# Kernel optimization log

Hardware: AMD Instinct MI355X
Metric: run time of the kernel (lower is better)

Reference implementation:

```python
import jax, jax.numpy as jnp
import numpy as np

# config
L, N, D, H, I = 4, 16, 64, 1024, 4096   # layers, heads, head_dim, hidden, intermediate
V, P = 50257, 8192                       # vocab, positions
B, S = 2, 2048                           # batch, seq
EPS = 1e-5


def setup_inputs() -> dict:
    key = jax.random.key(0)
    ks = jax.random.split(key, 20)
    std = 0.02
    inp = {
        "input_ids": jax.random.randint(ks[0], (B, S), 0, V),
        "position_ids": jnp.broadcast_to(jnp.arange(S), (B, S)),
        "wte": jax.random.normal(ks[1], (V, H), jnp.float32) * std,
        "wpe": jax.random.normal(ks[2], (P, H), jnp.float32) * std,
        # per-layer stacked params; torch Linear weights are (out, in)
        "ln1_w": jnp.ones((L, H), jnp.float32),
        "ln1_b": jnp.zeros((L, H), jnp.float32),
        "cattn_w": jax.random.normal(ks[3], (L, H + 2 * D, H), jnp.float32) * std,
        "cattn_b": jnp.zeros((L, H + 2 * D), jnp.float32),
        "cproj_w": jax.random.normal(ks[4], (L, H, H), jnp.float32) * std,
        "cproj_b": jnp.zeros((L, H), jnp.float32),
        "ln2_w": jnp.ones((L, H), jnp.float32),
        "ln2_b": jnp.zeros((L, H), jnp.float32),
        "fc_w": jax.random.normal(ks[5], (L, I, H), jnp.float32) * std,
        "fc_b": jnp.zeros((L, I), jnp.float32),
        "mproj_w": jax.random.normal(ks[6], (L, H, I), jnp.float32) * std,
        "mproj_b": jnp.zeros((L, H), jnp.float32),
        "lnf_w": jnp.ones((H,), jnp.float32),
        "lnf_b": jnp.zeros((H,), jnp.float32),
    }
    return inp


def _ln(x, w, b):
    mu = jnp.mean(x, axis=-1, keepdims=True)
    var = jnp.mean(jnp.square(x - mu), axis=-1, keepdims=True)
    return (x - mu) * jax.lax.rsqrt(var + EPS) * w + b


def _forward(input_ids, position_ids, wte, wpe, ln1_w, ln1_b, cattn_w, cattn_b,
             cproj_w, cproj_b, ln2_w, ln2_b, fc_w, fc_b, mproj_w, mproj_b,
             lnf_w, lnf_b):
    h = wte[input_ids] + wpe[position_ids]              # [B,S,H]
    b, s, _ = h.shape
    causal = jnp.tril(jnp.ones((s, s), bool))[None, :, None, :]   # [1,S,1,S] keep-mask
    neg = jnp.finfo(jnp.float32).min
    for l in range(L):
        # --- attention ---
        resid = h
        x = _ln(h, ln1_w[l], ln1_b[l])
        qkv = x @ cattn_w[l].T + cattn_b[l]             # [B,S,H+2D]
        q = qkv[..., :H].reshape(b, s, N, D)
        k = qkv[..., H:H + D]                           # [B,S,D] shared key head
        v = qkv[..., H + D:]                            # [B,S,D] shared value head
        unscale = float(l + 1)
        scale = 1.0 / (unscale * np.sqrt(D))
        scores = jnp.einsum('bsnd,btd->bsnt', q, k) * scale
        # upcast_masked_softmax: to fp32, re-multiply by unscale, mask, softmax
        scores = scores.astype(jnp.float32) * unscale
        scores = jnp.where(causal, scores, neg)
        attn = jax.nn.softmax(scores, axis=-1).astype(h.dtype)
        out = jnp.einsum('bsnt,btd->bsnd', attn, v).reshape(b, s, H)
        h = resid + (out @ cproj_w[l].T + cproj_b[l])
        # --- mlp ---
        resid = h
        x = _ln(h, ln2_w[l], ln2_b[l])
        x = jax.nn.gelu(x @ fc_w[l].T + fc_b[l], approximate=False)
        h = resid + (x @ mproj_w[l].T + mproj_b[l])
    return _ln(h, lnf_w, lnf_b)


def reference(input_ids, position_ids, wte, wpe, ln1_w, ln1_b, cattn_w, cattn_b,
              cproj_w, cproj_b, ln2_w, ln2_b, fc_w, fc_b, mproj_w, mproj_b,
              lnf_w, lnf_b):
    return _forward(input_ids, position_ids, wte, wpe, ln1_w, ln1_b, cattn_w,
                    cattn_b, cproj_w, cproj_b, ln2_w, ln2_b, fc_w, fc_b,
                    mproj_w, mproj_b, lnf_w, lnf_b)
```

## Files before the change

### kernel.cpp

```cpp
#include <hip/hip_runtime.h>
#include <math.h>

typedef __attribute__((ext_vector_type(8))) short short8;
typedef __attribute__((ext_vector_type(8))) __bf16 bf16x8;
typedef __attribute__((ext_vector_type(4))) float f32x4;

static constexpr int H = 1024, LNUM = 4, SEQ = 2048, BATCH = 2;
static constexpr int TOK = BATCH * SEQ;
static constexpr int NI = 4096, QKVD = H + 128;

__device__ __forceinline__ short f2bf(float f) {
  union { float f; unsigned u; } c; c.f = f;
  return (short)((c.u + 0x7fffu + ((c.u >> 16) & 1u)) >> 16);
}

__device__ __forceinline__ void gl_lds16(const short* g, short* l) {
  __builtin_amdgcn_global_load_lds(
      (const __attribute__((address_space(1))) unsigned*)g,
      (__attribute__((address_space(3))) unsigned*)l, 16, 0, 0);
}

#define MFMA16(a, b, c) __builtin_amdgcn_mfma_f32_16x16x32_bf16(a, b, c, 0, 0, 0)

__global__ __launch_bounds__(256) void embed_kernel(
    const int* __restrict__ ids, const int* __restrict__ pos,
    const float* __restrict__ wte, const float* __restrict__ wpe,
    float* __restrict__ h) {
  int i = blockIdx.x * 256 + threadIdx.x;
  int tok = i >> 10, d = i & 1023;
  h[i] = wte[(size_t)ids[tok] * H + d] + wpe[(size_t)pos[tok] * H + d];
}

__global__ __launch_bounds__(256) void cast_kernel(
    const float* __restrict__ src, short* __restrict__ dst) {
  int i = blockIdx.x * 256 + threadIdx.x;
  float4 v = ((const float4*)src)[i];
  union { short s[4]; uint2 u; } p;
  p.s[0] = f2bf(v.x); p.s[1] = f2bf(v.y); p.s[2] = f2bf(v.z); p.s[3] = f2bf(v.w);
  ((uint2*)dst)[i] = p.u;
}

template <bool BF16_OUT>
__global__ __launch_bounds__(256) void ln_kernel(
    const float* __restrict__ X, const float* __restrict__ w,
    const float* __restrict__ b, void* __restrict__ out) {
  int row = blockIdx.x;
  const float* x = X + (size_t)row * H;
  int tid = threadIdx.x, lane = tid & 63, wid = tid >> 6;
  float v[4];
#pragma unroll
  for (int i = 0; i < 4; i++) v[i] = x[tid + i * 256];
  float s = v[0] + v[1] + v[2] + v[3];
#pragma unroll
  for (int off = 32; off > 0; off >>= 1) s += __shfl_xor(s, off);
  __shared__ float red[8];
  if (lane == 0) red[wid] = s;
  __syncthreads();
  float mu = (red[0] + red[1] + red[2] + red[3]) * (1.0f / H);
  float q = 0.f;
#pragma unroll
  for (int i = 0; i < 4; i++) { float d = v[i] - mu; q += d * d; }
#pragma unroll
  for (int off = 32; off > 0; off >>= 1) q += __shfl_xor(q, off);
  if (lane == 0) red[4 + wid] = q;
  __syncthreads();
  float var = (red[4] + red[5] + red[6] + red[7]) * (1.0f / H);
  float inv = rsqrtf(var + 1e-5f);
#pragma unroll
  for (int i = 0; i < 4; i++) {
    int col = tid + i * 256;
    float r = (v[i] - mu) * inv * w[col] + b[col];
    if (BF16_OUT) ((short*)out)[(size_t)row * H + col] = f2bf(r);
    else          ((float*)out)[(size_t)row * H + col] = r;
  }
}

template <int MODE>
__global__ __launch_bounds__(256) void gemm_mfma(
    const short* __restrict__ A, const short* __restrict__ W,
    const float* __restrict__ bias, void* __restrict__ Cv,
    int M, int N, int K) {
  __shared__ short As[128 * 32];
  __shared__ short Bs[128 * 32];
  int tid = threadIdx.x, wave = tid >> 6, lane = tid & 63;
  int li = lane & 15, lg = lane >> 4;
  int row0 = blockIdx.y * 128, col0 = blockIdx.x * 128;
  int wm = (wave & 1) * 64, wn = (wave >> 1) * 64;
  f32x4 acc[4][4] = {};
  const short* Ab = A + (size_t)(row0 + (tid >> 2)) * K + (tid & 3) * 8;
  const short* Wb = W + (size_t)(col0 + (tid >> 2)) * K + (tid & 3) * 8;
  for (int k0 = 0; k0 < K; k0 += 32) {
    __syncthreads();
    gl_lds16(Ab + k0,            As + tid * 8);
    gl_lds16(Ab + k0 + 64 * K,   As + 2048 + tid * 8);
    gl_lds16(Wb + k0,            Bs + tid * 8);
    gl_lds16(Wb + k0 + 64 * K,   Bs + 2048 + tid * 8);
    __syncthreads();
    bf16x8 af[4], bfr[4];
#pragma unroll
    for (int i = 0; i < 4; ++i) {
      af[i]  = *(const bf16x8*)&As[(wm + i * 16 + li) * 32 + lg * 8];
      bfr[i] = *(const bf16x8*)&Bs[(wn + i * 16 + li) * 32 + lg * 8];
    }
#pragma unroll
    for (int i = 0; i < 4; ++i)
#pragma unroll
      for (int j = 0; j < 4; ++j) acc[i][j] = MFMA16(af[i], bfr[j], acc[i][j]);
  }
  float* Cf = (float*)Cv;
  short* Cs = (short*)Cv;
#pragma unroll
  for (int i = 0; i < 4; ++i) {
    int gr = row0 + wm + i * 16 + lg * 4;
#pragma unroll
    for (int j = 0; j < 4; ++j) {
      int gc = col0 + wn + j * 16 + li;
      float bv = bias[gc];
#pragma unroll
      for (int r = 0; r < 4; ++r) {
        float v = acc[i][j][r] + bv;
        size_t idx = (size_t)(gr + r) * N + gc;
        if (MODE == 1) {
          Cf[idx] += v;
        } else if (MODE == 2) {
          v = 0.5f * v * (1.0f + erff(v * 0.70710678118654752f));
          Cs[idx] = f2bf(v);
        } else {
          Cs[idx] = f2bf(v);
        }
      }
    }
  }
}

__global__ __launch_bounds__(256) void mqa_attn(
    const short* __restrict__ qkv, short* __restrict__ out) {
  int head = blockIdx.x, qt = blockIdx.y, b = blockIdx.z;
  int tid = threadIdx.x, wave = tid >> 6, lane = tid & 63;
  int li = lane & 15, lg = lane >> 4;

  __shared__ short Kc[64 * 72];
  __shared__ short VT[64 * 72];
  __shared__ short Ps[4 * 16 * 72];

  const size_t qrow0 = (size_t)(b * SEQ + qt * 64);
  bf16x8 qf[2];
  {
    const short* qp = qkv + (qrow0 + wave * 16 + li) * QKVD + head * 64 + lg * 8;
    qf[0] = *(const bf16x8*)(qp);
    qf[1] = *(const bf16x8*)(qp + 32);
  }
  f32x4 oacc[4] = {};
  float m_i[4], l_i[4];
#pragma unroll
  for (int r = 0; r < 4; ++r) { m_i[r] = -1e30f; l_i[r] = 0.f; }

  int t_ = tid >> 3, c_ = tid & 7;
  for (int j = 0; j <= qt; ++j) {
    __syncthreads();
    {
      const short* g0 = qkv + ((size_t)(b * SEQ + j * 64 + t_)) * QKVD;
      const short* g1 = g0 + 32 * QKVD;
      short8 k0 = *(const short8*)(g0 + 1024 + c_ * 8);
      short8 k1 = *(const short8*)(g1 + 1024 + c_ * 8);
      short8 v0 = *(const short8*)(g0 + 1088 + c_ * 8);
      short8 v1 = *(const short8*)(g1 + 1088 + c_ * 8);
      *(short8*)&Kc[t_ * 72 + c_ * 8] = k0;
      *(short8*)&Kc[(t_ + 32) * 72 + c_ * 8] = k1;
#pragma unroll
      for (int e = 0; e < 8; ++e) {
        VT[(c_ * 8 + e) * 72 + t_] = v0[e];
        VT[(c_ * 8 + e) * 72 + t_ + 32] = v1[e];
      }
    }
    __syncthreads();

    f32x4 s[4];
#pragma unroll
    for (int n = 0; n < 4; ++n) {
      bf16x8 kf0 = *(const bf16x8*)&Kc[(n * 16 + li) * 72 + lg * 8];
      bf16x8 kf1 = *(const bf16x8*)&Kc[(n * 16 + li) * 72 + 32 + lg * 8];
      f32x4 a = {};
      a = MFMA16(qf[0], kf0, a);
      a = MFMA16(qf[1], kf1, a);
      s[n] = a;
    }
    bool diag = (j == qt);
#pragma unroll
    for (int n = 0; n < 4; ++n)
#pragma unroll
      for (int r = 0; r < 4; ++r) {
        float v = s[n][r] * 0.125f;
        if (diag && (n * 16 + li) > (wave * 16 + lg * 4 + r)) v = -1e30f;
        s[n][r] = v;
      }
    float alpha[4];
#pragma unroll
    for (int r = 0; r < 4; ++r) {
      float mx = fmaxf(fmaxf(s[0][r], s[1][r]), fmaxf(s[2][r], s[3][r]));
#pragma unroll
      for (int off = 1; off < 16; off <<= 1) mx = fmaxf(mx, __shfl_xor(mx, off));
      float mn = fmaxf(m_i[r], mx);
      alpha[r] = __expf(m_i[r] - mn);
      m_i[r] = mn;
      float ps = 0.f;
#pragma unroll
      for (int n = 0; n < 4; ++n) {
        float p = __expf(s[n][r] - mn);
        s[n][r] = p;
        ps += p;
      }
#pragma unroll
      for (int off = 1; off < 16; off <<= 1) ps += __shfl_xor(ps, off);
      l_i[r] = l_i[r] * alpha[r] + ps;
    }
#pragma unroll
    for (int dn = 0; dn < 4; ++dn)
#pragma unroll
      for (int r = 0; r < 4; ++r) oacc[dn][r] *= alpha[r];
    short* pw = Ps + wave * 1152;
#pragma unroll
    for (int n = 0; n < 4; ++n)
#pragma unroll
      for (int r = 0; r < 4; ++r) pw[(lg * 4 + r) * 72 + n * 16 + li] = f2bf(s[n][r]);
#pragma unroll
    for (int ks = 0; ks < 2; ++ks) {
      bf16x8 pf = *(const bf16x8*)&pw[li * 72 + ks * 32 + lg * 8];
#pragma unroll
      for (int dn = 0; dn < 4; ++dn) {
        bf16x8 vf = *(const bf16x8*)&VT[(dn * 16 + li) * 72 + ks * 32 + lg * 8];
        oacc[dn] = MFMA16(pf, vf, oacc[dn]);
      }
    }
  }
#pragma unroll
  for (int r = 0; r < 4; ++r) {
    float inv = 1.0f / l_i[r];
    size_t row = (qrow0 + wave * 16 + lg * 4 + r) * H + head * 64;
#pragma unroll
    for (int dn = 0; dn < 4; ++dn) out[row + dn * 16 + li] = f2bf(oacc[dn][r] * inv);
  }
}

extern "C" void kernel_launch(void* const* d_in, const int* in_sizes, int n_in,
                              void* d_out, int out_size, void* d_ws, size_t ws_size,
                              hipStream_t stream) {
  const int*   input_ids    = (const int*)d_in[0];
  const int*   position_ids = (const int*)d_in[1];
  const float* wte     = (const float*)d_in[2];
  const float* wpe     = (const float*)d_in[3];
  const float* ln1_w   = (const float*)d_in[4];
  const float* ln1_b   = (const float*)d_in[5];
  const float* cattn_w = (const float*)d_in[6];
  const float* cattn_b = (const float*)d_in[7];
  const float* cproj_w = (const float*)d_in[8];
  const float* cproj_b = (const float*)d_in[9];
  const float* ln2_w   = (const float*)d_in[10];
  const float* ln2_b   = (const float*)d_in[11];
  const float* fc_w    = (const float*)d_in[12];
  const float* fc_b    = (const float*)d_in[13];
  const float* mproj_w = (const float*)d_in[14];
  const float* mproj_b = (const float*)d_in[15];
  const float* lnf_w   = (const float*)d_in[16];
  const float* lnf_b   = (const float*)d_in[17];

  float* h     = (float*)d_ws;
  short* xbf   = (short*)(h + (size_t)TOK * H);
  short* qkvbf = xbf + (size_t)TOK * H;
  short* fcbf  = qkvbf + (size_t)TOK * QKVD;
  short* wqkv  = fcbf + (size_t)TOK * NI;
  short* wcp   = wqkv + (size_t)QKVD * H;
  short* wfc   = wcp + (size_t)H * H;
  short* wmp   = wfc + (size_t)NI * H;

  embed_kernel<<<TOK * H / 256, 256, 0, stream>>>(input_ids, position_ids, wte, wpe, h);

  for (int l = 0; l < LNUM; l++) {
    cast_kernel<<<QKVD * H / 1024, 256, 0, stream>>>(cattn_w + (size_t)l * QKVD * H, wqkv);
    cast_kernel<<<H * H / 1024, 256, 0, stream>>>(cproj_w + (size_t)l * H * H, wcp);
    cast_kernel<<<NI * H / 1024, 256, 0, stream>>>(fc_w + (size_t)l * NI * H, wfc);
    cast_kernel<<<H * NI / 1024, 256, 0, stream>>>(mproj_w + (size_t)l * H * NI, wmp);

    ln_kernel<true><<<TOK, 256, 0, stream>>>(h, ln1_w + l * H, ln1_b + l * H, xbf);
    gemm_mfma<0><<<dim3(QKVD / 128, TOK / 128), 256, 0, stream>>>(
        xbf, wqkv, cattn_b + (size_t)l * QKVD, qkvbf, TOK, QKVD, H);
    mqa_attn<<<dim3(16, 32, BATCH), 256, 0, stream>>>(qkvbf, xbf);
    gemm_mfma<1><<<dim3(H / 128, TOK / 128), 256, 0, stream>>>(
        xbf, wcp, cproj_b + (size_t)l * H, h, TOK, H, H);
    ln_kernel<true><<<TOK, 256, 0, stream>>>(h, ln2_w + l * H, ln2_b + l * H, xbf);
    gemm_mfma<2><<<dim3(NI / 128, TOK / 128), 256, 0, stream>>>(
        xbf, wfc, fc_b + (size_t)l * NI, fcbf, TOK, NI, H);
    gemm_mfma<1><<<dim3(H / 128, TOK / 128), 256, 0, stream>>>(
        fcbf, wmp, mproj_b + (size_t)l * H, h, TOK, H, NI);
  }
  ln_kernel<false><<<TOK, 256, 0, stream>>>(h, lnf_w, lnf_b, d_out);
}
```

Measured before the change: 1.958 ms.

## Pre-transpose shared V, read K/V from global in attention, narrow GEMM tiles

Adds a kernel that writes the shared value head transposed into a workspace buffer once per layer. The attention kernel then reads K and V fragments directly from global memory (L2-resident) instead of staging them through LDS with block barriers, and walks query tiles heaviest-first to balance causal work. The smaller-N GEMMs (qkv, c_proj, mlp proj) switch to a 128x64 tile to launch more blocks on the many CUs. The risks are extra workspace use, uncoalesced strided K reads, and lower per-block MFMA reuse in the narrower GEMMs.

```diff
diff --git a/kernel.cpp b/kernel.cpp
--- a/kernel.cpp
+++ b/kernel.cpp
@@ -75,42 +75,69 @@
   }
 }
 
-template <int MODE>
+__global__ __launch_bounds__(256) void vtrans_kernel(
+    const short* __restrict__ qkv, short* __restrict__ vt) {
+  __shared__ short Vs[64 * 68];
+  int t0 = blockIdx.x * 64, b = blockIdx.y;
+  int tid = threadIdx.x;
+  int t = tid >> 2;
+#pragma unroll
+  for (int it = 0; it < 2; ++it) {
+    int seg = (tid & 3) + it * 4;
+    *(short8*)&Vs[t * 68 + seg * 8] =
+        *(const short8*)(qkv + ((size_t)(b * SEQ) + t0 + t) * QKVD + 1088 + seg * 8);
+  }
+  __syncthreads();
+  int tg = tid & 7;
+#pragma unroll
+  for (int it = 0; it < 2; ++it) {
+    int d = (tid >> 3) + it * 32;
+    short8 v;
+#pragma unroll
+    for (int e = 0; e < 8; ++e) v[e] = Vs[(tg * 8 + e) * 68 + d];
+    *(short8*)(vt + ((size_t)(b * 64) + d) * SEQ + t0 + tg * 8) = v;
+  }
+}
+
+template <int BN, int MODE>
 __global__ __launch_bounds__(256) void gemm_mfma(
     const short* __restrict__ A, const short* __restrict__ W,
     const float* __restrict__ bias, void* __restrict__ Cv,
     int M, int N, int K) {
   __shared__ short As[128 * 32];
-  __shared__ short Bs[128 * 32];
+  __shared__ short Bs[BN * 32];
+  constexpr int MI = (BN == 128) ? 4 : 2;
   int tid = threadIdx.x, wave = tid >> 6, lane = tid & 63;
   int li = lane & 15, lg = lane >> 4;
-  int row0 = blockIdx.y * 128, col0 = blockIdx.x * 128;
-  int wm = (wave & 1) * 64, wn = (wave >> 1) * 64;
-  f32x4 acc[4][4] = {};
+  int row0 = blockIdx.y * 128, col0 = blockIdx.x * BN;
+  int wm = (BN == 128) ? (wave & 1) * 64 : wave * 32;
+  int wn = (BN == 128) ? (wave >> 1) * 64 : 0;
+  f32x4 acc[MI][4] = {};
   const short* Ab = A + (size_t)(row0 + (tid >> 2)) * K + (tid & 3) * 8;
   const short* Wb = W + (size_t)(col0 + (tid >> 2)) * K + (tid & 3) * 8;
   for (int k0 = 0; k0 < K; k0 += 32) {
     __syncthreads();
-    gl_lds16(Ab + k0,            As + tid * 8);
-    gl_lds16(Ab + k0 + 64 * K,   As + 2048 + tid * 8);
-    gl_lds16(Wb + k0,            Bs + tid * 8);
-    gl_lds16(Wb + k0 + 64 * K,   Bs + 2048 + tid * 8);
+    gl_lds16(Ab + k0,          As + tid * 8);
+    gl_lds16(Ab + k0 + 64 * K, As + 2048 + tid * 8);
+    gl_lds16(Wb + k0,          Bs + tid * 8);
+    if (BN == 128) gl_lds16(Wb + k0 + 64 * K, Bs + 2048 + tid * 8);
     __syncthreads();
-    bf16x8 af[4], bfr[4];
-#pragma unroll
-    for (int i = 0; i < 4; ++i) {
-      af[i]  = *(const bf16x8*)&As[(wm + i * 16 + li) * 32 + lg * 8];
-      bfr[i] = *(const bf16x8*)&Bs[(wn + i * 16 + li) * 32 + lg * 8];
-    }
-#pragma unroll
-    for (int i = 0; i < 4; ++i)
+    bf16x8 af[MI], bfr[4];
+#pragma unroll
+    for (int i = 0; i < MI; ++i)
+      af[i] = *(const bf16x8*)&As[(wm + i * 16 + li) * 32 + lg * 8];
+#pragma unroll
+    for (int j = 0; j < 4; ++j)
+      bfr[j] = *(const bf16x8*)&Bs[(wn + j * 16 + li) * 32 + lg * 8];
+#pragma unroll
+    for (int i = 0; i < MI; ++i)
 #pragma unroll
       for (int j = 0; j < 4; ++j) acc[i][j] = MFMA16(af[i], bfr[j], acc[i][j]);
   }
   float* Cf = (float*)Cv;
   short* Cs = (short*)Cv;
 #pragma unroll
-  for (int i = 0; i < 4; ++i) {
+  for (int i = 0; i < MI; ++i) {
     int gr = row0 + wm + i * 16 + lg * 4;
 #pragma unroll
     for (int j = 0; j < 4; ++j) {
@@ -134,13 +161,13 @@
 }
 
 __global__ __launch_bounds__(256) void mqa_attn(
-    const short* __restrict__ qkv, short* __restrict__ out) {
-  int head = blockIdx.x, qt = blockIdx.y, b = blockIdx.z;
+    const short* __restrict__ qkv, const short* __restrict__ vt,
+    short* __restrict__ out) {
+  int qt = gridDim.x - 1 - blockIdx.x;
+  int head = blockIdx.y, b = blockIdx.z;
   int tid = threadIdx.x, wave = tid >> 6, lane = tid & 63;
   int li = lane & 15, lg = lane >> 4;
 
-  __shared__ short Kc[64 * 72];
-  __shared__ short VT[64 * 72];
   __shared__ short Ps[4 * 16 * 72];
 
   const size_t qrow0 = (size_t)(b * SEQ + qt * 64);
@@ -154,35 +181,18 @@
   float m_i[4], l_i[4];
 #pragma unroll
   for (int r = 0; r < 4; ++r) { m_i[r] = -1e30f; l_i[r] = 0.f; }
-
-  int t_ = tid >> 3, c_ = tid & 7;
+  short* pw = Ps + wave * 1152;
+
   for (int j = 0; j <= qt; ++j) {
-    __syncthreads();
-    {
-      const short* g0 = qkv + ((size_t)(b * SEQ + j * 64 + t_)) * QKVD;
-      const short* g1 = g0 + 32 * QKVD;
-      short8 k0 = *(const short8*)(g0 + 1024 + c_ * 8);
-      short8 k1 = *(const short8*)(g1 + 1024 + c_ * 8);
-      short8 v0 = *(const short8*)(g0 + 1088 + c_ * 8);
-      short8 v1 = *(const short8*)(g1 + 1088 + c_ * 8);
-      *(short8*)&Kc[t_ * 72 + c_ * 8] = k0;
-      *(short8*)&Kc[(t_ + 32) * 72 + c_ * 8] = k1;
-#pragma unroll
-      for (int e = 0; e < 8; ++e) {
-        VT[(c_ * 8 + e) * 72 + t_] = v0[e];
-        VT[(c_ * 8 + e) * 72 + t_ + 32] = v1[e];
-      }
-    }
-    __syncthreads();
-
+    const short* kb = qkv + ((size_t)(b * SEQ + j * 64)) * QKVD + 1024;
+    const short* vb = vt + (size_t)(b * 64) * SEQ + j * 64;
     f32x4 s[4];
 #pragma unroll
     for (int n = 0; n < 4; ++n) {
-      bf16x8 kf0 = *(const bf16x8*)&Kc[(n * 16 + li) * 72 + lg * 8];
-      bf16x8 kf1 = *(const bf16x8*)&Kc[(n * 16 + li) * 72 + 32 + lg * 8];
+      const short* kr = kb + (size_t)(n * 16 + li) * QKVD + lg * 8;
       f32x4 a = {};
-      a = MFMA16(qf[0], kf0, a);
-      a = MFMA16(qf[1], kf1, a);
+      a = MFMA16(qf[0], *(const bf16x8*)kr, a);
+      a = MFMA16(qf[1], *(const bf16x8*)(kr + 32), a);
       s[n] = a;
     }
     bool diag = (j == qt);
@@ -218,7 +228,6 @@
     for (int dn = 0; dn < 4; ++dn)
 #pragma unroll
       for (int r = 0; r < 4; ++r) oacc[dn][r] *= alpha[r];
-    short* pw = Ps + wave * 1152;
 #pragma unroll
     for (int n = 0; n < 4; ++n)
 #pragma unroll
@@ -228,7 +237,7 @@
       bf16x8 pf = *(const bf16x8*)&pw[li * 72 + ks * 32 + lg * 8];
 #pragma unroll
       for (int dn = 0; dn < 4; ++dn) {
-        bf16x8 vf = *(const bf16x8*)&VT[(dn * 16 + li) * 72 + ks * 32 + lg * 8];
+        bf16x8 vf = *(const bf16x8*)(vb + (size_t)(dn * 16 + li) * SEQ + ks * 32 + lg * 8);
         oacc[dn] = MFMA16(pf, vf, oacc[dn]);
       }
     }
@@ -272,6 +281,7 @@
   short* wcp   = wqkv + (size_t)QKVD * H;
   short* wfc   = wcp + (size_t)H * H;
   short* wmp   = wfc + (size_t)NI * H;
+  short* vt    = wmp + (size_t)H * NI;
 
   embed_kernel<<<TOK * H / 256, 256, 0, stream>>>(input_ids, position_ids, wte, wpe, h);
 
@@ -282,15 +292,16 @@
     cast_kernel<<<H * NI / 1024, 256, 0, stream>>>(mproj_w + (size_t)l * H * NI, wmp);
 
     ln_kernel<true><<<TOK, 256, 0, stream>>>(h, ln1_w + l * H, ln1_b + l * H, xbf);
-    gemm_mfma<0><<<dim3(QKVD / 128, TOK / 128), 256, 0, stream>>>(
+    gemm_mfma<64, 0><<<dim3(QKVD / 64, TOK / 128), 256, 0, stream>>>(
         xbf, wqkv, cattn_b + (size_t)l * QKVD, qkvbf, TOK, QKVD, H);
-    mqa_attn<<<dim3(16, 32, BATCH), 256, 0, stream>>>(qkvbf, xbf);
-    gemm_mfma<1><<<dim3(H / 128, TOK / 128), 256, 0, stream>>>(
+    vtrans_kernel<<<dim3(SEQ / 64, BATCH), 256, 0, stream>>>(qkvbf, vt);
+    mqa_attn<<<dim3(32, 16, BATCH), 256, 0, stream>>>(qkvbf, vt, xbf);
+    gemm_mfma<64, 1><<<dim3(H / 64, TOK / 128), 256, 0, stream>>>(
         xbf, wcp, cproj_b + (size_t)l * H, h, TOK, H, H);
     ln_kernel<true><<<TOK, 256, 0, stream>>>(h, ln2_w + l * H, ln2_b + l * H, xbf);
-    gemm_mfma<2><<<dim3(NI / 128, TOK / 128), 256, 0, stream>>>(
+    gemm_mfma<128, 2><<<dim3(NI / 128, TOK / 128), 256, 0, stream>>>(
         xbf, wfc, fc_b + (size_t)l * NI, fcbf, TOK, NI, H);
-    gemm_mfma<1><<<dim3(H / 128, TOK / 128), 256, 0, stream>>>(
+    gemm_mfma<64, 1><<<dim3(H / 64, TOK / 128), 256, 0, stream>>>(
         fcbf, wmp, mproj_b + (size_t)l * H, h, TOK, H, NI);
   }
   ln_kernel<false><<<TOK, 256, 0, stream>>>(h, lnf_w, lnf_b, d_out);
```

Result: slower. 2.195 ms (+12.1%).
